# Kernel tuning notes

Hardware: AMD Instinct MI355X
Metric: run time of the kernel (lower is better)

Reference implementation:

```python
import jax, jax.numpy as jnp
import numpy as np

BINS = 10
MIU = 0.02
SHAPE = (8, 160, 160, 36)  # (batch, h, w, num_anchors*4)


def setup_inputs() -> dict:
    key = jax.random.key(0)
    k1, k2, k3 = jax.random.split(key, 3)
    delta_targets = jax.random.normal(k1, SHAPE, dtype=jnp.float32)
    deltas = jax.random.normal(k2, SHAPE, dtype=jnp.float32)
    delta_weights = (jax.random.uniform(k3, SHAPE) < 0.3).astype(jnp.float32)
    return {"delta_targets": delta_targets, "deltas": deltas, "delta_weights": delta_weights}


def reference(delta_targets, deltas, delta_weights):
    # bin edges: [0, 0.1, ..., 0.9, 1.0 + 1e-6]
    edges = jnp.arange(BINS + 1, dtype=jnp.float32) / BINS
    edges = edges.at[BINS].add(1e-6)

    diff = deltas - delta_targets
    denom = jnp.sqrt(diff * diff + MIU * MIU)
    asl1 = denom - MIU                       # authentic smooth L1 (ASL1)
    grads = jnp.abs(diff / denom)            # gradient norm, in [0, 1)

    total_num = jnp.maximum(jnp.sum(delta_weights), 1.0)
    valid = delta_weights > 0

    # per-element bin index: edges[i] <= g < edges[i+1]
    idx = jnp.clip(jnp.digitize(grads.ravel(), edges) - 1, 0, BINS - 1)
    # histogram of valid elements per bin (replaces the 10 masked reduce_sums)
    counts = jax.ops.segment_sum(valid.ravel().astype(jnp.float32), idx, num_segments=BINS)

    n_nonempty = jnp.sum(counts > 0).astype(jnp.float32)
    per_bin_w = jnp.where(counts > 0, total_num / jnp.maximum(counts, 1.0), 0.0)

    beta = jnp.where(valid, per_bin_w[idx].reshape(grads.shape), 0.0)
    beta = beta / jnp.maximum(n_nonempty, 1.0)

    return asl1 * beta / total_num
```

## Files before the change

### kernel.cpp

```cpp
#include <hip/hip_runtime.h>

#define NBINS 10
#define TPB 256
#define PBLOCKS 1024
#define PROW 16
#define PACKED_OFF (1 << 18)

typedef unsigned long long u64;

__device__ __forceinline__ unsigned int pack_elem(float a, float b, float w,
                                                  float& wsum, u64& h) {
    float d = b - a;
    float dn = sqrtf(d * d + 0.0004f);
    float g = fabsf(d / dn);
    wsum += w;
    bool valid = w > 0.0f;
    int bin = 0;
    bin += g >= 0.1f; bin += g >= 0.2f; bin += g >= 0.3f;
    bin += g >= 0.4f; bin += g >= 0.5f; bin += g >= 0.6f;
    bin += g >= 0.7f; bin += g >= 0.8f; bin += g >= 0.9f;
    h += (u64)valid << (bin * 6);
    int idx = valid ? bin : NBINS;
    float asl1 = dn - 0.02f;
    return (__float_as_uint(asl1) & 0xFFFFFFF0u) | (unsigned int)idx;
}

__global__ __launch_bounds__(TPB) void ghmr_pass1(
    const float4* __restrict__ dt4, const float4* __restrict__ dl4,
    const float4* __restrict__ dw4, uint4* __restrict__ packed,
    float* __restrict__ partials, int n4)
{
    const int tid = blockIdx.x * TPB + threadIdx.x;
    const int stride = PBLOCKS * TPB;

    float wsum = 0.0f;
    u64 h = 0ULL;

    for (int q = tid; q < n4; q += stride) {
        float4 a = dt4[q];
        float4 b = dl4[q];
        float4 w = dw4[q];
        uint4 p;
        p.x = pack_elem(a.x, b.x, w.x, wsum, h);
        p.y = pack_elem(a.y, b.y, w.y, wsum, h);
        p.z = pack_elem(a.z, b.z, w.z, wsum, h);
        p.w = pack_elem(a.w, b.w, w.w, wsum, h);
        packed[q] = p;
    }

    int cnt[NBINS];
#pragma unroll
    for (int k = 0; k < NBINS; ++k) cnt[k] = (int)((h >> (6 * k)) & 63ULL);

#pragma unroll
    for (int off = 32; off > 0; off >>= 1) {
        wsum += __shfl_down(wsum, off);
#pragma unroll
        for (int k = 0; k < NBINS; ++k) cnt[k] += __shfl_down(cnt[k], off);
    }

    __shared__ float s_w[4];
    __shared__ int   s_c[4][NBINS];
    const int lane = threadIdx.x & 63;
    const int wave = threadIdx.x >> 6;
    if (lane == 0) {
        s_w[wave] = wsum;
#pragma unroll
        for (int k = 0; k < NBINS; ++k) s_c[wave][k] = cnt[k];
    }
    __syncthreads();
    if (threadIdx.x == 0)
        partials[blockIdx.x * PROW] = s_w[0] + s_w[1] + s_w[2] + s_w[3];
    if (threadIdx.x < NBINS) {
        int tc = s_c[0][threadIdx.x] + s_c[1][threadIdx.x] +
                 s_c[2][threadIdx.x] + s_c[3][threadIdx.x];
        partials[blockIdx.x * PROW + 1 + threadIdx.x] = (float)tc;
    }
}

__global__ __launch_bounds__(TPB) void ghmr_pass2(
    const uint4* __restrict__ packed, const float* __restrict__ partials,
    float4* __restrict__ out4, int n4)
{
    float acc[NBINS + 1];
#pragma unroll
    for (int k = 0; k <= NBINS; ++k) acc[k] = 0.0f;
    for (int r = threadIdx.x; r < PBLOCKS; r += TPB) {
        const float* row = partials + r * PROW;
#pragma unroll
        for (int k = 0; k <= NBINS; ++k) acc[k] += row[k];
    }
#pragma unroll
    for (int off = 32; off > 0; off >>= 1)
#pragma unroll
        for (int k = 0; k <= NBINS; ++k) acc[k] += __shfl_down(acc[k], off);

    __shared__ float s_acc[4][NBINS + 1];
    __shared__ float s_sb[NBINS + 1];
    const int lane = threadIdx.x & 63;
    const int wave = threadIdx.x >> 6;
    if (lane == 0)
#pragma unroll
        for (int k = 0; k <= NBINS; ++k) s_acc[wave][k] = acc[k];
    __syncthreads();

    if (threadIdx.x == 0) {
        float total = fmaxf(s_acc[0][0] + s_acc[1][0] + s_acc[2][0] + s_acc[3][0], 1.0f);
        float cf[NBINS];
        int nne = 0;
#pragma unroll
        for (int b = 0; b < NBINS; ++b) {
            cf[b] = s_acc[0][b + 1] + s_acc[1][b + 1] + s_acc[2][b + 1] + s_acc[3][b + 1];
            nne += (cf[b] > 0.0f) ? 1 : 0;
        }
        float nnef = fmaxf((float)nne, 1.0f);
#pragma unroll
        for (int b = 0; b < NBINS; ++b) {
            float pbw = (cf[b] > 0.0f) ? (total / fmaxf(cf[b], 1.0f)) : 0.0f;
            s_sb[b] = pbw / nnef / total;
        }
        s_sb[NBINS] = 0.0f;
    }
    __syncthreads();

    const int tid = blockIdx.x * TPB + threadIdx.x;
    const int stride = PBLOCKS * TPB;
    for (int q = tid; q < n4; q += stride) {
        uint4 p = packed[q];
        float4 r;
        r.x = __uint_as_float(p.x & 0xFFFFFFF0u) * s_sb[p.x & 0xFu];
        r.y = __uint_as_float(p.y & 0xFFFFFFF0u) * s_sb[p.y & 0xFu];
        r.z = __uint_as_float(p.z & 0xFFFFFFF0u) * s_sb[p.z & 0xFu];
        r.w = __uint_as_float(p.w & 0xFFFFFFF0u) * s_sb[p.w & 0xFu];
        out4[q] = r;
    }
}

__global__ void ghmr_tail(const float* __restrict__ dt, const float* __restrict__ dl,
                          const float* __restrict__ dw, const float* __restrict__ partials,
                          float* __restrict__ out, int n, int n4)
{
    float acc[NBINS + 1];
    for (int k = 0; k <= NBINS; ++k) acc[k] = 0.0f;
    for (int r = 0; r < PBLOCKS; ++r)
        for (int k = 0; k <= NBINS; ++k) acc[k] += partials[r * PROW + k];
    float total = fmaxf(acc[0], 1.0f);
    int nne = 0;
    for (int b = 0; b < NBINS; ++b) nne += (acc[b + 1] > 0.0f) ? 1 : 0;
    float nnef = fmaxf((float)nne, 1.0f);
    for (int i = (n4 << 2) + threadIdx.x; i < n; i += blockDim.x) {
        float d = dl[i] - dt[i];
        float dn = sqrtf(d * d + 0.0004f);
        float g = fabsf(d / dn);
        int bin = 0;
        bin += g >= 0.1f; bin += g >= 0.2f; bin += g >= 0.3f;
        bin += g >= 0.4f; bin += g >= 0.5f; bin += g >= 0.6f;
        bin += g >= 0.7f; bin += g >= 0.8f; bin += g >= 0.9f;
        float cf = acc[bin + 1];
        float pbw = (cf > 0.0f) ? (total / fmaxf(cf, 1.0f)) : 0.0f;
        out[i] = (dw[i] > 0.0f) ? (dn - 0.02f) * (pbw / nnef / total) : 0.0f;
    }
}

extern "C" void kernel_launch(void* const* d_in, const int* in_sizes, int n_in,
                              void* d_out, int out_size, void* d_ws, size_t ws_size,
                              hipStream_t stream) {
    const float* dt = (const float*)d_in[0];
    const float* dl = (const float*)d_in[1];
    const float* dw = (const float*)d_in[2];
    float* out = (float*)d_out;
    float* partials = (float*)d_ws;
    uint4* packed = (uint4*)((float*)d_ws + PACKED_OFF);
    const int n = in_sizes[0];
    const int n4 = n >> 2;

    ghmr_pass1<<<PBLOCKS, TPB, 0, stream>>>(
        (const float4*)dt, (const float4*)dl, (const float4*)dw,
        packed, partials, n4);
    ghmr_pass2<<<PBLOCKS, TPB, 0, stream>>>(
        packed, partials, (float4*)out, n4);
    if (n & 3)
        ghmr_tail<<<1, 256, 0, stream>>>(dt, dl, dw, partials, out, n, n4);
}
```

Measured before the change: 133.6 us.

## Move histogram finalization into a single-block kernel, double pass grid size

Each pass2 block used to reduce all per-block partials redundantly before doing its elementwise work. A new single-block finalize kernel now computes the per-bin scale factors once and writes them to workspace, and pass2 only loads these 11 floats into shared memory. The block count for both passes doubles to 2048. This adds an extra kernel launch and a serial dependency in exchange for removing the redundant reduction from every pass2 block.

```diff
diff --git a/kernel.cpp b/kernel.cpp
--- a/kernel.cpp
+++ b/kernel.cpp
@@ -2,8 +2,9 @@
 
 #define NBINS 10
 #define TPB 256
-#define PBLOCKS 1024
+#define PBLOCKS 2048
 #define PROW 16
+#define PARAMS_OFF (PBLOCKS * PROW)
 #define PACKED_OFF (1 << 18)
 
 typedef unsigned long long u64;
@@ -78,9 +79,8 @@
     }
 }
 
-__global__ __launch_bounds__(TPB) void ghmr_pass2(
-    const uint4* __restrict__ packed, const float* __restrict__ partials,
-    float4* __restrict__ out4, int n4)
+__global__ __launch_bounds__(TPB) void ghmr_finalize(
+    const float* __restrict__ partials, float* __restrict__ params)
 {
     float acc[NBINS + 1];
 #pragma unroll
@@ -96,7 +96,6 @@
         for (int k = 0; k <= NBINS; ++k) acc[k] += __shfl_down(acc[k], off);
 
     __shared__ float s_acc[4][NBINS + 1];
-    __shared__ float s_sb[NBINS + 1];
     const int lane = threadIdx.x & 63;
     const int wave = threadIdx.x >> 6;
     if (lane == 0)
@@ -117,10 +116,18 @@
 #pragma unroll
         for (int b = 0; b < NBINS; ++b) {
             float pbw = (cf[b] > 0.0f) ? (total / fmaxf(cf[b], 1.0f)) : 0.0f;
-            s_sb[b] = pbw / nnef / total;
+            params[b] = pbw / nnef / total;
         }
-        s_sb[NBINS] = 0.0f;
+        params[NBINS] = 0.0f;
     }
+}
+
+__global__ __launch_bounds__(TPB) void ghmr_pass2(
+    const uint4* __restrict__ packed, const float* __restrict__ params,
+    float4* __restrict__ out4, int n4)
+{
+    __shared__ float s_sb[NBINS + 1];
+    if (threadIdx.x <= NBINS) s_sb[threadIdx.x] = params[threadIdx.x];
     __syncthreads();
 
     const int tid = blockIdx.x * TPB + threadIdx.x;
@@ -137,17 +144,9 @@
 }
 
 __global__ void ghmr_tail(const float* __restrict__ dt, const float* __restrict__ dl,
-                          const float* __restrict__ dw, const float* __restrict__ partials,
+                          const float* __restrict__ dw, const float* __restrict__ params,
                           float* __restrict__ out, int n, int n4)
 {
-    float acc[NBINS + 1];
-    for (int k = 0; k <= NBINS; ++k) acc[k] = 0.0f;
-    for (int r = 0; r < PBLOCKS; ++r)
-        for (int k = 0; k <= NBINS; ++k) acc[k] += partials[r * PROW + k];
-    float total = fmaxf(acc[0], 1.0f);
-    int nne = 0;
-    for (int b = 0; b < NBINS; ++b) nne += (acc[b + 1] > 0.0f) ? 1 : 0;
-    float nnef = fmaxf((float)nne, 1.0f);
     for (int i = (n4 << 2) + threadIdx.x; i < n; i += blockDim.x) {
         float d = dl[i] - dt[i];
         float dn = sqrtf(d * d + 0.0004f);
@@ -156,9 +155,7 @@
         bin += g >= 0.1f; bin += g >= 0.2f; bin += g >= 0.3f;
         bin += g >= 0.4f; bin += g >= 0.5f; bin += g >= 0.6f;
         bin += g >= 0.7f; bin += g >= 0.8f; bin += g >= 0.9f;
-        float cf = acc[bin + 1];
-        float pbw = (cf > 0.0f) ? (total / fmaxf(cf, 1.0f)) : 0.0f;
-        out[i] = (dw[i] > 0.0f) ? (dn - 0.02f) * (pbw / nnef / total) : 0.0f;
+        out[i] = (dw[i] > 0.0f) ? (dn - 0.02f) * params[bin] : 0.0f;
     }
 }
 
@@ -170,6 +167,7 @@
     const float* dw = (const float*)d_in[2];
     float* out = (float*)d_out;
     float* partials = (float*)d_ws;
+    float* params = (float*)d_ws + PARAMS_OFF;
     uint4* packed = (uint4*)((float*)d_ws + PACKED_OFF);
     const int n = in_sizes[0];
     const int n4 = n >> 2;
@@ -177,8 +175,9 @@
     ghmr_pass1<<<PBLOCKS, TPB, 0, stream>>>(
         (const float4*)dt, (const float4*)dl, (const float4*)dw,
         packed, partials, n4);
+    ghmr_finalize<<<1, TPB, 0, stream>>>(partials, params);
     ghmr_pass2<<<PBLOCKS, TPB, 0, stream>>>(
-        packed, partials, (float4*)out, n4);
+        packed, params, (float4*)out, n4);
     if (n & 3)
-        ghmr_tail<<<1, 256, 0, stream>>>(dt, dl, dw, partials, out, n, n4);
+        ghmr_tail<<<1, 256, 0, stream>>>(dt, dl, dw, params, out, n, n4);
 }
```

New measurement: 137.4 us. +2.9%, slower.

## Write ASL1 to output in pass1 and stash 4-bit bin indices separately

Applied to the files above, without the earlier changes.

Pass1 now writes the smooth-L1 value directly into the output buffer and stores bin indices as packed 4-bit nibbles in a small u16 array, instead of a packed uint4 intermediate. Pass2 reads the nibbles plus the output, scales in place and writes back. The block count is doubled and an occupancy hint is added to the launch bounds. Total memory traffic is about the same or slightly higher, but precision no longer depends on mantissa truncation.

```diff
diff --git a/kernel.cpp b/kernel.cpp
--- a/kernel.cpp
+++ b/kernel.cpp
@@ -2,14 +2,16 @@
 
 #define NBINS 10
 #define TPB 256
-#define PBLOCKS 1024
+#define PBLOCKS 2048
 #define PROW 16
-#define PACKED_OFF (1 << 18)
+#define BINS_OFF (1 << 18)
 
 typedef unsigned long long u64;
+typedef unsigned short u16;
 
-__device__ __forceinline__ unsigned int pack_elem(float a, float b, float w,
-                                                  float& wsum, u64& h) {
+__device__ __forceinline__ float p1_elem(float a, float b, float w,
+                                         float& wsum, u64& h,
+                                         unsigned int& nib, int shift) {
     float d = b - a;
     float dn = sqrtf(d * d + 0.0004f);
     float g = fabsf(d / dn);
@@ -20,15 +22,14 @@
     bin += g >= 0.4f; bin += g >= 0.5f; bin += g >= 0.6f;
     bin += g >= 0.7f; bin += g >= 0.8f; bin += g >= 0.9f;
     h += (u64)valid << (bin * 6);
-    int idx = valid ? bin : NBINS;
-    float asl1 = dn - 0.02f;
-    return (__float_as_uint(asl1) & 0xFFFFFFF0u) | (unsigned int)idx;
+    nib |= (unsigned int)(valid ? bin : NBINS) << shift;
+    return dn - 0.02f;
 }
 
-__global__ __launch_bounds__(TPB) void ghmr_pass1(
+__global__ __launch_bounds__(TPB, 8) void ghmr_pass1(
     const float4* __restrict__ dt4, const float4* __restrict__ dl4,
-    const float4* __restrict__ dw4, uint4* __restrict__ packed,
-    float* __restrict__ partials, int n4)
+    const float4* __restrict__ dw4, float4* __restrict__ out4,
+    u16* __restrict__ bins, float* __restrict__ partials, int n4)
 {
     const int tid = blockIdx.x * TPB + threadIdx.x;
     const int stride = PBLOCKS * TPB;
@@ -40,12 +41,14 @@
         float4 a = dt4[q];
         float4 b = dl4[q];
         float4 w = dw4[q];
-        uint4 p;
-        p.x = pack_elem(a.x, b.x, w.x, wsum, h);
-        p.y = pack_elem(a.y, b.y, w.y, wsum, h);
-        p.z = pack_elem(a.z, b.z, w.z, wsum, h);
-        p.w = pack_elem(a.w, b.w, w.w, wsum, h);
-        packed[q] = p;
+        unsigned int nib = 0;
+        float4 r;
+        r.x = p1_elem(a.x, b.x, w.x, wsum, h, nib, 0);
+        r.y = p1_elem(a.y, b.y, w.y, wsum, h, nib, 4);
+        r.z = p1_elem(a.z, b.z, w.z, wsum, h, nib, 8);
+        r.w = p1_elem(a.w, b.w, w.w, wsum, h, nib, 12);
+        out4[q] = r;
+        bins[q] = (u16)nib;
     }
 
     int cnt[NBINS];
@@ -78,8 +81,8 @@
     }
 }
 
-__global__ __launch_bounds__(TPB) void ghmr_pass2(
-    const uint4* __restrict__ packed, const float* __restrict__ partials,
+__global__ __launch_bounds__(TPB, 8) void ghmr_pass2(
+    const u16* __restrict__ bins, const float* __restrict__ partials,
     float4* __restrict__ out4, int n4)
 {
     float acc[NBINS + 1];
@@ -126,13 +129,13 @@
     const int tid = blockIdx.x * TPB + threadIdx.x;
     const int stride = PBLOCKS * TPB;
     for (int q = tid; q < n4; q += stride) {
-        uint4 p = packed[q];
-        float4 r;
-        r.x = __uint_as_float(p.x & 0xFFFFFFF0u) * s_sb[p.x & 0xFu];
-        r.y = __uint_as_float(p.y & 0xFFFFFFF0u) * s_sb[p.y & 0xFu];
-        r.z = __uint_as_float(p.z & 0xFFFFFFF0u) * s_sb[p.z & 0xFu];
-        r.w = __uint_as_float(p.w & 0xFFFFFFF0u) * s_sb[p.w & 0xFu];
-        out4[q] = r;
+        unsigned int p = bins[q];
+        float4 v = out4[q];
+        v.x *= s_sb[p & 0xFu];
+        v.y *= s_sb[(p >> 4) & 0xFu];
+        v.z *= s_sb[(p >> 8) & 0xFu];
+        v.w *= s_sb[(p >> 12) & 0xFu];
+        out4[q] = v;
     }
 }
 
@@ -170,15 +173,15 @@
     const float* dw = (const float*)d_in[2];
     float* out = (float*)d_out;
     float* partials = (float*)d_ws;
-    uint4* packed = (uint4*)((float*)d_ws + PACKED_OFF);
+    u16* bins = (u16*)((float*)d_ws + BINS_OFF);
     const int n = in_sizes[0];
     const int n4 = n >> 2;
 
     ghmr_pass1<<<PBLOCKS, TPB, 0, stream>>>(
         (const float4*)dt, (const float4*)dl, (const float4*)dw,
-        packed, partials, n4);
+        (float4*)out, bins, partials, n4);
     ghmr_pass2<<<PBLOCKS, TPB, 0, stream>>>(
-        packed, partials, (float4*)out, n4);
+        bins, partials, (float4*)out, n4);
     if (n & 3)
         ghmr_tail<<<1, 256, 0, stream>>>(dt, dl, dw, partials, out, n, n4);
 }
```

After: 140.5 us. +5.2%, slower.
